# Performance work log

Hardware: AMD Instinct MI355X
Metric: run time of the kernel (lower is better)

The kernel has to match this reference:

```python
import jax, jax.numpy as jnp
import numpy as np

B, C, H, W = 8, 512, 64, 64
HEADS, GROUPS, EPS = 4, 32, 1e-5


def setup_inputs() -> dict:
    key = jax.random.key(0)
    ks = jax.random.split(key, 7)
    s = 0.02
    return {
        "x": jax.random.normal(ks[0], (B, C, H, W), dtype=jnp.float32),
        "gn_w": jnp.ones((C,), dtype=jnp.float32),
        "gn_b": jnp.zeros((C,), dtype=jnp.float32),
        "qkv_w": jax.random.normal(ks[1], (3 * C, C), dtype=jnp.float32) * s,
        "qkv_b": jnp.zeros((3 * C,), dtype=jnp.float32),
        "proj_w": jax.random.normal(ks[2], (C, C), dtype=jnp.float32) * s,
        "proj_b": jnp.zeros((C,), dtype=jnp.float32),
    }


def reference(x, gn_w, gn_b, qkv_w, qkv_b, proj_w, proj_b):
    b, c, h, w = x.shape
    d = c // HEADS  # per-head channel dim
    n = h * w
    # GroupNorm(32, C)
    xg = x.reshape(b, GROUPS, -1)
    mu = xg.mean(axis=-1, keepdims=True)
    var = xg.var(axis=-1, keepdims=True)
    hn = ((xg - mu) * jax.lax.rsqrt(var + EPS)).reshape(b, c, h, w)
    hn = hn * gn_w[:, None, None] + gn_b[:, None, None]
    # 1x1 conv qkv: [3C, C] contraction over channels
    qkv = jnp.einsum('oc,bchw->bohw', qkv_w, hn) + qkv_b[:, None, None]
    qkv = qkv.reshape(b, 3, HEADS, d, n)
    q, k, v = qkv[:, 0], qkv[:, 1], qkv[:, 2]  # each [b, heads, d, n]
    # NOTE: as in the source, q @ k^T contracts over spatial dim -> [b,heads,d,d]
    attn = jnp.einsum('bhdn,bhen->bhde', q, k) * (d ** -0.5)
    attn = jax.nn.softmax(attn, axis=-1)
    out = jnp.einsum('bhde,bhen->bhdn', attn, v).reshape(b, c, h, w)
    out = jnp.einsum('oc,bchw->bohw', proj_w, out) + proj_b[:, None, None]
    return x + out
```

## Files before the change

### kernel.cpp

```cpp
#include <hip/hip_runtime.h>
#include <hip/hip_bf16.h>

typedef __hip_bfloat16 bf16;
typedef __bf16 v8bf __attribute__((ext_vector_type(8)));
typedef float  v4f  __attribute__((ext_vector_type(4)));

struct __align__(8) bf16x4 { bf16 x, y, z, w; };

__device__ __forceinline__ bf16 f2b(float v) { return __float2bfloat16(v); }

#define NSP 4096
#define CCH 512

__device__ __forceinline__ void async_cp16(const bf16* g, __bf16* l) {
    __builtin_amdgcn_global_load_lds(
        (const __attribute__((address_space(1))) unsigned int*)(unsigned long long)g,
        (__attribute__((address_space(3))) unsigned int*)(unsigned int)(unsigned long long)l,
        16, 0, 0);
}

__global__ __launch_bounds__(256) void wconv_kernel(const float* __restrict__ src,
                                                    bf16* __restrict__ dst, int n4) {
    int i = blockIdx.x * 256 + threadIdx.x;
    if (i < n4) {
        float4 v = ((const float4*)src)[i];
        bf16x4 o = { f2b(v.x), f2b(v.y), f2b(v.z), f2b(v.w) };
        ((bf16x4*)dst)[i] = o;
    }
}

__global__ __launch_bounds__(256) void gn_stats_kernel(const float* __restrict__ x,
                                                       float* __restrict__ stats) {
    int blk = blockIdx.x;
    int b = blk >> 5, g = blk & 31;
    size_t base = ((size_t)(b * CCH + g * 16)) * NSP;
    const float4* xp4 = (const float4*)(x + base);
    int t = threadIdx.x;
    float s = 0.f, s2 = 0.f;
    for (int i = t; i < 16384; i += 256) {
        float4 v = xp4[i];
        s  += v.x + v.y + v.z + v.w;
        s2 += v.x * v.x + v.y * v.y + v.z * v.z + v.w * v.w;
    }
    for (int off = 32; off > 0; off >>= 1) {
        s  += __shfl_down(s, off);
        s2 += __shfl_down(s2, off);
    }
    __shared__ float red[8];
    int wid = t >> 6, lid = t & 63;
    if (lid == 0) { red[wid] = s; red[wid + 4] = s2; }
    __syncthreads();
    if (t == 0) {
        float ts  = red[0] + red[1] + red[2] + red[3];
        float ts2 = red[4] + red[5] + red[6] + red[7];
        float mean = ts * (1.f / 65536.f);
        float var  = ts2 * (1.f / 65536.f) - mean * mean;
        stats[blk * 2]     = mean;
        stats[blk * 2 + 1] = rsqrtf(var + 1e-5f);
    }
}

__global__ __launch_bounds__(256) void gn_norm_t_kernel(const float* __restrict__ x,
                                                        const float* __restrict__ gw,
                                                        const float* __restrict__ gb,
                                                        const float* __restrict__ stats,
                                                        bf16* __restrict__ hnT) {
    __shared__ float sT[64][65];
    int n0 = blockIdx.x * 64, c0 = blockIdx.y * 64, b = blockIdx.z;
    int t = threadIdx.x;
    int cl = t >> 4, nl4 = (t & 15) << 2;
#pragma unroll
    for (int it = 0; it < 4; ++it) {
        int crow = cl + it * 16;
        int c = c0 + crow;
        int bg = b * 32 + (c >> 4);
        float mean = stats[bg * 2], rstd = stats[bg * 2 + 1];
        float wsc = gw[c] * rstd;
        float bb  = gb[c] - mean * wsc;
        float4 v = *(const float4*)&x[((long)b * CCH + c) * NSP + n0 + nl4];
        sT[crow][nl4 + 0] = v.x * wsc + bb;
        sT[crow][nl4 + 1] = v.y * wsc + bb;
        sT[crow][nl4 + 2] = v.z * wsc + bb;
        sT[crow][nl4 + 3] = v.w * wsc + bb;
    }
    __syncthreads();
    int nl = t >> 4, cl4 = (t & 15) << 2;
#pragma unroll
    for (int it = 0; it < 4; ++it) {
        int nrow = nl + it * 16;
        bf16x4 ov = { f2b(sT[cl4 + 0][nrow]), f2b(sT[cl4 + 1][nrow]),
                      f2b(sT[cl4 + 2][nrow]), f2b(sT[cl4 + 3][nrow]) };
        *(bf16x4*)&hnT[((long)b * NSP + n0 + nrow) * CCH + c0 + cl4] = ov;
    }
}

__device__ __forceinline__ void gemm_core(const bf16* __restrict__ A, long as,
                                          const bf16* __restrict__ B, long bs,
                                          int K, v4f acc[4][4],
                                          __bf16* sA, __bf16* sB) {
    int t = threadIdx.x;
    int lane = t & 63, wv = t >> 6;
    int wr = wv >> 1, wc = wv & 1;
    int lq = lane & 15, quad = lane >> 4;
    int r0 = wv * 16 + (lane >> 2);
    int koff = (lane & 3) * 8;
    __bf16* ldsA0 = sA + wv * 512 + lane * 8;
    __bf16* ldsA1 = ldsA0 + 2048;
    __bf16* ldsB0 = sB + wv * 512 + lane * 8;
    __bf16* ldsB1 = ldsB0 + 2048;
    const __bf16* aBase = sA + (wr * 64) * 32;
    const __bf16* bBase = sB + (wc * 64) * 32;

    for (int k0 = 0; k0 < K; k0 += 32) {
        __syncthreads();
        async_cp16(A + (long)r0 * as + k0 + koff,        ldsA0);
        async_cp16(A + (long)(r0 + 64) * as + k0 + koff, ldsA1);
        async_cp16(B + (long)r0 * bs + k0 + koff,        ldsB0);
        async_cp16(B + (long)(r0 + 64) * bs + k0 + koff, ldsB1);
        __syncthreads();
        v8bf a[4], bf[4];
#pragma unroll
        for (int i = 0; i < 4; ++i)
            a[i] = *(const v8bf*)(aBase + (i * 16 + lq) * 32 + quad * 8);
#pragma unroll
        for (int j = 0; j < 4; ++j)
            bf[j] = *(const v8bf*)(bBase + (j * 16 + lq) * 32 + quad * 8);
#pragma unroll
        for (int i = 0; i < 4; ++i)
#pragma unroll
            for (int j = 0; j < 4; ++j)
                acc[i][j] = __builtin_amdgcn_mfma_f32_16x16x32_bf16(a[i], bf[j], acc[i][j], 0, 0, 0);
    }
}

__device__ __forceinline__ void gemm256_core(const bf16* __restrict__ A, long lda,
                                             const bf16* __restrict__ B, long ldb,
                                             int K, v4f acc[8][4], char* sLds) {
    const int t = threadIdx.x;
    const int lane = t & 63, wv = t >> 6;
    const int wm = wv >> 2, wn = wv & 3;
    const int lq = lane & 15, quad = lane >> 4;
    const int xsw = (lq & 7) << 4;
    const int kq0 = ((quad << 4)) ^ xsw;
    const int kq1 = (64 | (quad << 4)) ^ xsw;
    const int aRow0 = (wm * 128 + lq) << 7;
    const int bRow0 = (wn * 64 + lq) << 7;
    const int NT = K >> 6;

    auto STAGE = [&](const bf16* mb, long ld, int ldsbyte, int ktile, int h) {
#pragma unroll
        for (int s = 0; s < 2; ++s) {
            int L = (s << 13) + (t << 4);
            int row = L >> 7;
            int kb = (L & 127) ^ ((row & 7) << 4);
            const char* g = (const char*)(mb + (long)(h * 128 + row) * ld + (long)ktile * 64);
            async_cp16((const bf16*)(g + kb),
                       (__bf16*)(sLds + ldsbyte + (h << 14) + L));
        }
    };

    STAGE(B, ldb, 32768, 0, 0);
    STAGE(B, ldb, 32768, 0, 1);
    STAGE(A, lda, 0,     0, 0);
    STAGE(A, lda, 0,     0, 1);
    if (NT > 1) {
        STAGE(B, ldb, 65536 + 32768, 1, 0);
        STAGE(B, ldb, 65536 + 32768, 1, 1);
        asm volatile("s_waitcnt vmcnt(4)" ::: "memory");
    } else {
        asm volatile("s_waitcnt vmcnt(0)" ::: "memory");
    }
    __builtin_amdgcn_s_barrier();
    asm volatile("" ::: "memory");

    for (int kt = 0; kt < NT; ++kt) {
        const int cb = (kt & 1) << 16;
        const int nb = cb ^ 65536;
        const int bufA = cb, bufB = cb | 32768;
        v8bf a[4][2], b0[2][2], b1[2][2];

#pragma unroll
        for (int ii = 0; ii < 4; ++ii) {
            a[ii][0] = *(const v8bf*)(sLds + bufA + aRow0 + ((ii * 16) << 7) + kq0);
            a[ii][1] = *(const v8bf*)(sLds + bufA + aRow0 + ((ii * 16) << 7) + kq1);
        }
#pragma unroll
        for (int jj = 0; jj < 2; ++jj) {
            b0[jj][0] = *(const v8bf*)(sLds + bufB + bRow0 + ((jj * 16) << 7) + kq0);
            b0[jj][1] = *(const v8bf*)(sLds + bufB + bRow0 + ((jj * 16) << 7) + kq1);
        }
        if (kt + 1 < NT) STAGE(A, lda, nb, kt + 1, 0);
        __builtin_amdgcn_s_setprio(1);
#pragma unroll
        for (int ii = 0; ii < 4; ++ii)
#pragma unroll
            for (int jj = 0; jj < 2; ++jj) {
                acc[ii][jj] = __builtin_amdgcn_mfma_f32_16x16x32_bf16(a[ii][0], b0[jj][0], acc[ii][jj], 0, 0, 0);
                acc[ii][jj] = __builtin_amdgcn_mfma_f32_16x16x32_bf16(a[ii][1], b0[jj][1], acc[ii][jj], 0, 0, 0);
            }
        __builtin_amdgcn_s_setprio(0);
        __builtin_amdgcn_s_barrier();
        asm volatile("" ::: "memory");

#pragma unroll
        for (int jj = 0; jj < 2; ++jj) {
            b1[jj][0] = *(const v8bf*)(sLds + bufB + bRow0 + ((32 + jj * 16) << 7) + kq0);
            b1[jj][1] = *(const v8bf*)(sLds + bufB + bRow0 + ((32 + jj * 16) << 7) + kq1);
        }
        if (kt + 1 < NT) STAGE(A, lda, nb, kt + 1, 1);
        __builtin_amdgcn_s_setprio(1);
#pragma unroll
        for (int ii = 0; ii < 4; ++ii)
#pragma unroll
            for (int jj = 0; jj < 2; ++jj) {
                acc[ii][2 + jj] = __builtin_amdgcn_mfma_f32_16x16x32_bf16(a[ii][0], b1[jj][0], acc[ii][2 + jj], 0, 0, 0);
                acc[ii][2 + jj] = __builtin_amdgcn_mfma_f32_16x16x32_bf16(a[ii][1], b1[jj][1], acc[ii][2 + jj], 0, 0, 0);
            }
        __builtin_amdgcn_s_setprio(0);
        __builtin_amdgcn_s_barrier();
        asm volatile("" ::: "memory");

#pragma unroll
        for (int ii = 0; ii < 4; ++ii) {
            a[ii][0] = *(const v8bf*)(sLds + bufA + aRow0 + ((64 + ii * 16) << 7) + kq0);
            a[ii][1] = *(const v8bf*)(sLds + bufA + aRow0 + ((64 + ii * 16) << 7) + kq1);
        }
        if (kt + 2 < NT) STAGE(B, ldb, bufB, kt + 2, 0);
        __builtin_amdgcn_s_setprio(1);
#pragma unroll
        for (int ii = 0; ii < 4; ++ii)
#pragma unroll
            for (int jj = 0; jj < 2; ++jj) {
                acc[4 + ii][2 + jj] = __builtin_amdgcn_mfma_f32_16x16x32_bf16(a[ii][0], b1[jj][0], acc[4 + ii][2 + jj], 0, 0, 0);
                acc[4 + ii][2 + jj] = __builtin_amdgcn_mfma_f32_16x16x32_bf16(a[ii][1], b1[jj][1], acc[4 + ii][2 + jj], 0, 0, 0);
            }
        __builtin_amdgcn_s_setprio(0);
        __builtin_amdgcn_s_barrier();
        asm volatile("" ::: "memory");

        if (kt + 2 < NT) STAGE(B, ldb, bufB, kt + 2, 1);
        __builtin_amdgcn_s_setprio(1);
#pragma unroll
        for (int ii = 0; ii < 4; ++ii)
#pragma unroll
            for (int jj = 0; jj < 2; ++jj) {
                acc[4 + ii][jj] = __builtin_amdgcn_mfma_f32_16x16x32_bf16(a[ii][0], b0[jj][0], acc[4 + ii][jj], 0, 0, 0);
                acc[4 + ii][jj] = __builtin_amdgcn_mfma_f32_16x16x32_bf16(a[ii][1], b0[jj][1], acc[4 + ii][jj], 0, 0, 0);
            }
        __builtin_amdgcn_s_setprio(0);
        if (kt + 2 < NT) asm volatile("s_waitcnt vmcnt(4)" ::: "memory");
        else             asm volatile("s_waitcnt vmcnt(0)" ::: "memory");
        __builtin_amdgcn_s_barrier();
        asm volatile("" ::: "memory");
    }
}

__global__ __launch_bounds__(512, 2) void qkv_gemm_kernel(const bf16* __restrict__ hnT,
                                                          const bf16* __restrict__ qkv_wb,
                                                          const float* __restrict__ qkv_b,
                                                          bf16* __restrict__ qkbuf,
                                                          bf16* __restrict__ vT) {
    __shared__ __align__(16) char sLds[131072];
    int n0 = blockIdx.x * 256, o0 = blockIdx.y * 256, b = blockIdx.z;
    v4f acc[8][4] = {};
    gemm256_core(hnT + ((long)b * NSP + n0) * CCH, CCH,
                 qkv_wb + (long)o0 * CCH, CCH, CCH, acc, sLds);
    int t = threadIdx.x, lane = t & 63, wv = t >> 6, wm = wv >> 2, wn = wv & 3;
    int lq = lane & 15, quad = lane >> 4;
    if (o0 < 1024) {
#pragma unroll
        for (int j = 0; j < 4; ++j) {
            int o = o0 + wn * 64 + j * 16 + lq;
            float bias = qkv_b[o];
#pragma unroll
            for (int i = 0; i < 8; ++i) {
                int n = n0 + wm * 128 + i * 16 + quad * 4;
                v4f v = acc[i][j];
                bf16x4 ov = { f2b(v[0] + bias), f2b(v[1] + bias),
                              f2b(v[2] + bias), f2b(v[3] + bias) };
                *(bf16x4*)&qkbuf[((long)b * 1024 + o) * NSP + n] = ov;
            }
        }
    } else {
#pragma unroll
        for (int j = 0; j < 4; ++j) {
            int e = o0 - 1024 + wn * 64 + j * 16 + lq;
            float bias = qkv_b[1024 + e];
#pragma unroll
            for (int i = 0; i < 8; ++i) {
                int n = n0 + wm * 128 + i * 16 + quad * 4;
                v4f v = acc[i][j];
#pragma unroll
                for (int r = 0; r < 4; ++r)
                    vT[((long)b * NSP + n + r) * CCH + e] = f2b(v[r] + bias);
            }
        }
    }
}

__global__ __launch_bounds__(256) void qk_gemm_kernel(const bf16* __restrict__ qkbuf,
                                                      float* __restrict__ P_part) {
    __shared__ __align__(16) __bf16 sA[128 * 32];
    __shared__ __align__(16) __bf16 sB[128 * 32];
    int s = blockIdx.x, bh = blockIdx.y;
    int b = bh >> 2, h = bh & 3;
    const bf16* q  = qkbuf + ((long)b * 1024 + h * 128) * NSP + s * 512;
    const bf16* kk = qkbuf + ((long)b * 1024 + 512 + h * 128) * NSP + s * 512;
    v4f acc[4][4] = {};
    gemm_core(q, NSP, kk, NSP, 512, acc, sA, sB);
    float* Pp = P_part + ((long)s * 32 + bh) * 16384;
    int t = threadIdx.x, lane = t & 63, wv = t >> 6, wr = wv >> 1, wc = wv & 1;
    int lq = lane & 15, quad = lane >> 4;
#pragma unroll
    for (int j = 0; j < 4; ++j) {
        int e = wc * 64 + j * 16 + lq;
#pragma unroll
        for (int i = 0; i < 4; ++i) {
            int d = wr * 64 + i * 16 + quad * 4;
            v4f v = acc[i][j];
#pragma unroll
            for (int r = 0; r < 4; ++r) Pp[(long)(d + r) * 128 + e] = v[r];
        }
    }
}

__global__ __launch_bounds__(128) void softmax_kernel(const float* __restrict__ P_part,
                                                      bf16* __restrict__ Pb) {
    int row = blockIdx.x;
    int bh = row >> 7, d = row & 127;
    int t = threadIdx.x;
    float v = 0.f;
#pragma unroll
    for (int s = 0; s < 8; ++s)
        v += P_part[((long)s * 32 + bh) * 16384 + (long)d * 128 + t];
    v *= 0.08838834764831845f;
    float m = v;
    for (int off = 32; off > 0; off >>= 1) m = fmaxf(m, __shfl_down(m, off));
    __shared__ float sm[2];
    if ((t & 63) == 0) sm[t >> 6] = m;
    __syncthreads();
    m = fmaxf(sm[0], sm[1]);
    float e = __expf(v - m);
    float ssum = e;
    for (int off = 32; off > 0; off >>= 1) ssum += __shfl_down(ssum, off);
    __shared__ float ss[2];
    if ((t & 63) == 0) ss[t >> 6] = ssum;
    __syncthreads();
    ssum = ss[0] + ss[1];
    Pb[(long)row * 128 + t] = f2b(e / ssum);
}

__global__ __launch_bounds__(256) void pv_gemm_kernel(const bf16* __restrict__ Pb,
                                                      const bf16* __restrict__ vT,
                                                      bf16* __restrict__ attT) {
    __shared__ __align__(16) char sV[2][32768];
    int ng = blockIdx.x, bh = blockIdx.y;
    int b = bh >> 2, h = bh & 3;
    int t = threadIdx.x, lane = t & 63, wv = t >> 6, wr = wv >> 1, wc = wv & 1;
    int lq = lane & 15, quad = lane >> 4;

    auto STAGEV = [&](int n0, int buf) {
#pragma unroll
        for (int s = 0; s < 8; ++s) {
            int L = (s << 12) + (t << 4);
            int row = L >> 8;
            int col = (L & 255) ^ ((row & 7) << 4);
            async_cp16((const bf16*)((const char*)(vT + ((long)b * NSP + n0 + row) * CCH + h * 128) + col),
                       (__bf16*)(&sV[buf][0] + L));
        }
    };

    int n00 = ng * 256;
    STAGEV(n00, 0);
    v8bf a[4][4];
    const char* Pp = (const char*)(Pb + (long)bh * 16384);
#pragma unroll
    for (int i = 0; i < 4; ++i)
#pragma unroll
        for (int ks = 0; ks < 4; ++ks)
            a[i][ks] = *(const v8bf*)(Pp + ((wr * 64 + i * 16 + lq) << 8) + (ks << 6) + (quad << 4));
    STAGEV(n00 + 128, 1);
    asm volatile("s_waitcnt vmcnt(8)" ::: "memory");
    __syncthreads();

#pragma unroll
    for (int nt = 0; nt < 2; ++nt) {
        int n0 = n00 + nt * 128;
        const char* base = &sV[nt][0];
        v4f acc[4][4] = {};
#pragma unroll
        for (int ks = 0; ks < 4; ++ks) {
            v8bf bv[4];
#pragma unroll
            for (int j = 0; j < 4; ++j) {
                int r = wc * 64 + j * 16 + lq;
                bv[j] = *(const v8bf*)(base + (r << 8) + (((ks << 6) + (quad << 4)) ^ ((r & 7) << 4)));
            }
#pragma unroll
            for (int i = 0; i < 4; ++i)
#pragma unroll
                for (int j = 0; j < 4; ++j)
                    acc[i][j] = __builtin_amdgcn_mfma_f32_16x16x32_bf16(a[i][ks], bv[j], acc[i][j], 0, 0, 0);
        }
#pragma unroll
        for (int j = 0; j < 4; ++j) {
            int n = n0 + wc * 64 + j * 16 + lq;
#pragma unroll
            for (int i = 0; i < 4; ++i) {
                int d = wr * 64 + i * 16 + quad * 4;
                v4f v = acc[i][j];
                bf16x4 ov = { f2b(v[0]), f2b(v[1]), f2b(v[2]), f2b(v[3]) };
                *(bf16x4*)&attT[((long)b * NSP + n) * CCH + h * 128 + d] = ov;
            }
        }
        if (nt == 0) {
            asm volatile("s_waitcnt vmcnt(0)" ::: "memory");
            __syncthreads();
        }
    }
}

__global__ __launch_bounds__(512, 2) void proj_gemm_kernel(const bf16* __restrict__ attT,
                                                           const bf16* __restrict__ proj_wb,
                                                           const float* __restrict__ proj_b,
                                                           const float* __restrict__ x,
                                                           float* __restrict__ out) {
    __shared__ __align__(16) char sLds[131072];
    int n0 = blockIdx.x * 256, c0 = blockIdx.y * 256, b = blockIdx.z;
    v4f acc[8][4] = {};
    gemm256_core(attT + ((long)b * NSP + n0) * CCH, CCH,
                 proj_wb + (long)c0 * CCH, CCH, CCH, acc, sLds);
    int t = threadIdx.x, lane = t & 63, wv = t >> 6, wm = wv >> 2, wn = wv & 3;
    int lq = lane & 15, quad = lane >> 4;
#pragma unroll
    for (int j = 0; j < 4; ++j) {
        int c = c0 + wn * 64 + j * 16 + lq;
        float bias = proj_b[c];
#pragma unroll
        for (int i = 0; i < 8; ++i) {
            int n = n0 + wm * 128 + i * 16 + quad * 4;
            long idx = ((long)b * CCH + c) * NSP + n;
            float4 r = *(const float4*)&x[idx];
            v4f v = acc[i][j];
            float4 ov = { v[0] + bias + r.x, v[1] + bias + r.y,
                          v[2] + bias + r.z, v[3] + bias + r.w };
            *(float4*)&out[idx] = ov;
        }
    }
}

extern "C" void kernel_launch(void* const* d_in, const int* in_sizes, int n_in,
                              void* d_out, int out_size, void* d_ws, size_t ws_size,
                              hipStream_t stream) {
    const float* x      = (const float*)d_in[0];
    const float* gn_w   = (const float*)d_in[1];
    const float* gn_b   = (const float*)d_in[2];
    const float* qkv_w  = (const float*)d_in[3];
    const float* qkv_b  = (const float*)d_in[4];
    const float* proj_w = (const float*)d_in[5];
    const float* proj_b = (const float*)d_in[6];
    float* out = (float*)d_out;

    char* ws = (char*)d_ws;
    bf16*  hnT    = (bf16*)ws;
    float* P_part = (float*)ws;
    bf16*  attT   = (bf16*)ws;
    bf16*  qkbuf  = (bf16*)(ws + 33554432);
    bf16*  vT     = (bf16*)(ws + 100663296);
    bf16*  Pb     = (bf16*)(ws + 134217728);
    float* stats  = (float*)(ws + 135266304);
    bf16*  qkv_wb = (bf16*)(ws + 135270400);
    bf16*  proj_wb= (bf16*)(ws + 136843264);

    wconv_kernel<<<768, 256, 0, stream>>>(qkv_w, qkv_wb, 196608);
    wconv_kernel<<<256, 256, 0, stream>>>(proj_w, proj_wb, 65536);
    gn_stats_kernel<<<256, 256, 0, stream>>>(x, stats);
    gn_norm_t_kernel<<<dim3(64, 8, 8), 256, 0, stream>>>(x, gn_w, gn_b, stats, hnT);
    qkv_gemm_kernel<<<dim3(16, 6, 8), 512, 0, stream>>>(hnT, qkv_wb, qkv_b, qkbuf, vT);
    qk_gemm_kernel<<<dim3(8, 32), 256, 0, stream>>>(qkbuf, P_part);
    softmax_kernel<<<4096, 128, 0, stream>>>(P_part, Pb);
    pv_gemm_kernel<<<dim3(16, 32), 256, 0, stream>>>(Pb, vT, attT);
    proj_gemm_kernel<<<dim3(16, 2, 8), 512, 0, stream>>>(attT, proj_wb, proj_b, x, out);
}
```

Measured before the change: 307.4 us.

## Make QKV GEMM persistent with three tiles per block and cross-tile prefetch

The QKV GEMM launch changes from a 768-block grid to 256 persistent blocks, each computing three consecutive 256x256 output tiles. The K-loop pipeline is inlined and keeps prefetching across tile boundaries, so the next tile's first A/B k-tiles load while the current tile finishes. The goal is to remove per-tile pipeline warm-up and drain and to avoid a partial last wave across the 256 CUs. The cost is a longer serial chain per block, and the epilogue stores are not overlapped with the loads.

```diff
diff --git a/kernel.cpp b/kernel.cpp
--- a/kernel.cpp
+++ b/kernel.cpp
@@ -261,38 +261,188 @@
                                                           bf16* __restrict__ qkbuf,
                                                           bf16* __restrict__ vT) {
     __shared__ __align__(16) char sLds[131072];
-    int n0 = blockIdx.x * 256, o0 = blockIdx.y * 256, b = blockIdx.z;
+    const int p = blockIdx.x;
+    const int t = threadIdx.x;
+    const int lane = t & 63, wv = t >> 6;
+    const int wm = wv >> 2, wn = wv & 3;
+    const int lq = lane & 15, quad = lane >> 4;
+    const int xsw = (lq & 7) << 4;
+    const int kq0 = ((quad << 4)) ^ xsw;
+    const int kq1 = (64 | (quad << 4)) ^ xsw;
+    const int aRow0 = (wm * 128 + lq) << 7;
+    const int bRow0 = (wn * 64 + lq) << 7;
+
+    auto decodeA = [&](int l) -> const bf16* {
+        int n0 = (l & 15) << 8; int b = (l >> 4) / 6;
+        return hnT + ((long)b * NSP + n0) * CCH;
+    };
+    auto decodeB = [&](int l) -> const bf16* {
+        int o0 = ((l >> 4) % 6) << 8;
+        return qkv_wb + (long)o0 * CCH;
+    };
+
+    auto STAGE = [&](const bf16* mb, int ldsbyte, int ktile, int h) {
+#pragma unroll
+        for (int s = 0; s < 2; ++s) {
+            int L = (s << 13) + (t << 4);
+            int row = L >> 7;
+            int kb = (L & 127) ^ ((row & 7) << 4);
+            const char* g = (const char*)(mb + (long)(h * 128 + row) * CCH + (long)ktile * 64);
+            async_cp16((const bf16*)(g + kb),
+                       (__bf16*)(sLds + ldsbyte + (h << 14) + L));
+        }
+    };
+
+    const int l0 = p * 3;
+    const bf16* Acur = decodeA(l0);
+    const bf16* Bcur = decodeB(l0);
+    const bf16* Anxt = decodeA(l0 + 1);
+    const bf16* Bnxt = decodeB(l0 + 1);
+
     v4f acc[8][4] = {};
-    gemm256_core(hnT + ((long)b * NSP + n0) * CCH, CCH,
-                 qkv_wb + (long)o0 * CCH, CCH, CCH, acc, sLds);
-    int t = threadIdx.x, lane = t & 63, wv = t >> 6, wm = wv >> 2, wn = wv & 3;
-    int lq = lane & 15, quad = lane >> 4;
-    if (o0 < 1024) {
-#pragma unroll
-        for (int j = 0; j < 4; ++j) {
-            int o = o0 + wn * 64 + j * 16 + lq;
-            float bias = qkv_b[o];
-#pragma unroll
-            for (int i = 0; i < 8; ++i) {
-                int n = n0 + wm * 128 + i * 16 + quad * 4;
-                v4f v = acc[i][j];
-                bf16x4 ov = { f2b(v[0] + bias), f2b(v[1] + bias),
-                              f2b(v[2] + bias), f2b(v[3] + bias) };
-                *(bf16x4*)&qkbuf[((long)b * 1024 + o) * NSP + n] = ov;
-            }
-        }
-    } else {
-#pragma unroll
-        for (int j = 0; j < 4; ++j) {
-            int e = o0 - 1024 + wn * 64 + j * 16 + lq;
-            float bias = qkv_b[1024 + e];
-#pragma unroll
-            for (int i = 0; i < 8; ++i) {
-                int n = n0 + wm * 128 + i * 16 + quad * 4;
-                v4f v = acc[i][j];
-#pragma unroll
-                for (int r = 0; r < 4; ++r)
-                    vT[((long)b * NSP + n + r) * CCH + e] = f2b(v[r] + bias);
+
+    STAGE(Bcur, 32768, 0, 0);
+    STAGE(Bcur, 32768, 0, 1);
+    STAGE(Acur, 0,     0, 0);
+    STAGE(Acur, 0,     0, 1);
+    STAGE(Bcur, 65536 + 32768, 1, 0);
+    STAGE(Bcur, 65536 + 32768, 1, 1);
+    asm volatile("s_waitcnt vmcnt(4)" ::: "memory");
+    __builtin_amdgcn_s_barrier();
+    asm volatile("" ::: "memory");
+
+    for (int ti = 0; ti < 3; ++ti) {
+        for (int kt = 0; kt < 8; ++kt) {
+            const int cb = (kt & 1) << 16;
+            const int nb = cb ^ 65536;
+            const int bufA = cb, bufB = cb | 32768;
+            v8bf a[4][2], b0[2][2], b1[2][2];
+
+            const bf16* As = (kt < 7) ? Acur : Anxt;
+            const int   Akt = (kt < 7) ? kt + 1 : 0;
+            const bool  doA = !(ti == 2 && kt == 7);
+            const bf16* Bs = (kt < 6) ? Bcur : Bnxt;
+            const int   Bkt = (kt < 6) ? kt + 2 : kt - 6;
+            const bool  doB = !(ti == 2 && kt >= 6);
+
+#pragma unroll
+            for (int ii = 0; ii < 4; ++ii) {
+                a[ii][0] = *(const v8bf*)(sLds + bufA + aRow0 + ((ii * 16) << 7) + kq0);
+                a[ii][1] = *(const v8bf*)(sLds + bufA + aRow0 + ((ii * 16) << 7) + kq1);
+            }
+#pragma unroll
+            for (int jj = 0; jj < 2; ++jj) {
+                b0[jj][0] = *(const v8bf*)(sLds + bufB + bRow0 + ((jj * 16) << 7) + kq0);
+                b0[jj][1] = *(const v8bf*)(sLds + bufB + bRow0 + ((jj * 16) << 7) + kq1);
+            }
+            if (doA) STAGE(As, nb, Akt, 0);
+            __builtin_amdgcn_s_setprio(1);
+#pragma unroll
+            for (int ii = 0; ii < 4; ++ii)
+#pragma unroll
+                for (int jj = 0; jj < 2; ++jj) {
+                    acc[ii][jj] = __builtin_amdgcn_mfma_f32_16x16x32_bf16(a[ii][0], b0[jj][0], acc[ii][jj], 0, 0, 0);
+                    acc[ii][jj] = __builtin_amdgcn_mfma_f32_16x16x32_bf16(a[ii][1], b0[jj][1], acc[ii][jj], 0, 0, 0);
+                }
+            __builtin_amdgcn_s_setprio(0);
+            __builtin_amdgcn_s_barrier();
+            asm volatile("" ::: "memory");
+
+#pragma unroll
+            for (int jj = 0; jj < 2; ++jj) {
+                b1[jj][0] = *(const v8bf*)(sLds + bufB + bRow0 + ((32 + jj * 16) << 7) + kq0);
+                b1[jj][1] = *(const v8bf*)(sLds + bufB + bRow0 + ((32 + jj * 16) << 7) + kq1);
+            }
+            if (doA) STAGE(As, nb, Akt, 1);
+            __builtin_amdgcn_s_setprio(1);
+#pragma unroll
+            for (int ii = 0; ii < 4; ++ii)
+#pragma unroll
+                for (int jj = 0; jj < 2; ++jj) {
+                    acc[ii][2 + jj] = __builtin_amdgcn_mfma_f32_16x16x32_bf16(a[ii][0], b1[jj][0], acc[ii][2 + jj], 0, 0, 0);
+                    acc[ii][2 + jj] = __builtin_amdgcn_mfma_f32_16x16x32_bf16(a[ii][1], b1[jj][1], acc[ii][2 + jj], 0, 0, 0);
+                }
+            __builtin_amdgcn_s_setprio(0);
+            __builtin_amdgcn_s_barrier();
+            asm volatile("" ::: "memory");
+
+#pragma unroll
+            for (int ii = 0; ii < 4; ++ii) {
+                a[ii][0] = *(const v8bf*)(sLds + bufA + aRow0 + ((64 + ii * 16) << 7) + kq0);
+                a[ii][1] = *(const v8bf*)(sLds + bufA + aRow0 + ((64 + ii * 16) << 7) + kq1);
+            }
+            if (doB) STAGE(Bs, bufB, Bkt, 0);
+            __builtin_amdgcn_s_setprio(1);
+#pragma unroll
+            for (int ii = 0; ii < 4; ++ii)
+#pragma unroll
+                for (int jj = 0; jj < 2; ++jj) {
+                    acc[4 + ii][2 + jj] = __builtin_amdgcn_mfma_f32_16x16x32_bf16(a[ii][0], b1[jj][0], acc[4 + ii][2 + jj], 0, 0, 0);
+                    acc[4 + ii][2 + jj] = __builtin_amdgcn_mfma_f32_16x16x32_bf16(a[ii][1], b1[jj][1], acc[4 + ii][2 + jj], 0, 0, 0);
+                }
+            __builtin_amdgcn_s_setprio(0);
+            __builtin_amdgcn_s_barrier();
+            asm volatile("" ::: "memory");
+
+            if (doB) STAGE(Bs, bufB, Bkt, 1);
+            __builtin_amdgcn_s_setprio(1);
+#pragma unroll
+            for (int ii = 0; ii < 4; ++ii)
+#pragma unroll
+                for (int jj = 0; jj < 2; ++jj) {
+                    acc[4 + ii][jj] = __builtin_amdgcn_mfma_f32_16x16x32_bf16(a[ii][0], b0[jj][0], acc[4 + ii][jj], 0, 0, 0);
+                    acc[4 + ii][jj] = __builtin_amdgcn_mfma_f32_16x16x32_bf16(a[ii][1], b0[jj][1], acc[4 + ii][jj], 0, 0, 0);
+                }
+            __builtin_amdgcn_s_setprio(0);
+            if (doB) asm volatile("s_waitcnt vmcnt(4)" ::: "memory");
+            else     asm volatile("s_waitcnt vmcnt(0)" ::: "memory");
+            __builtin_amdgcn_s_barrier();
+            asm volatile("" ::: "memory");
+        }
+
+        {
+            int l = l0 + ti;
+            int n0 = (l & 15) << 8;
+            int oc = l >> 4;
+            int o0 = (oc % 6) << 8;
+            int b  = oc / 6;
+            if (o0 < 1024) {
+#pragma unroll
+                for (int j = 0; j < 4; ++j) {
+                    int o = o0 + wn * 64 + j * 16 + lq;
+                    float bias = qkv_b[o];
+#pragma unroll
+                    for (int i = 0; i < 8; ++i) {
+                        int n = n0 + wm * 128 + i * 16 + quad * 4;
+                        v4f v = acc[i][j];
+                        bf16x4 ov = { f2b(v[0] + bias), f2b(v[1] + bias),
+                                      f2b(v[2] + bias), f2b(v[3] + bias) };
+                        *(bf16x4*)&qkbuf[((long)b * 1024 + o) * NSP + n] = ov;
+                    }
+                }
+            } else {
+#pragma unroll
+                for (int j = 0; j < 4; ++j) {
+                    int e = o0 - 1024 + wn * 64 + j * 16 + lq;
+                    float bias = qkv_b[1024 + e];
+#pragma unroll
+                    for (int i = 0; i < 8; ++i) {
+                        int n = n0 + wm * 128 + i * 16 + quad * 4;
+                        v4f v = acc[i][j];
+#pragma unroll
+                        for (int r = 0; r < 4; ++r)
+                            vT[((long)b * NSP + n + r) * CCH + e] = f2b(v[r] + bias);
+                    }
+                }
+            }
+            if (ti < 2) {
+#pragma unroll
+                for (int i = 0; i < 8; ++i)
+#pragma unroll
+                    for (int j = 0; j < 4; ++j)
+                        acc[i][j] = (v4f){0.f, 0.f, 0.f, 0.f};
+                Acur = Anxt; Bcur = Bnxt;
+                if (ti == 0) { Anxt = decodeA(l0 + 2); Bnxt = decodeB(l0 + 2); }
             }
         }
     }
@@ -476,7 +626,7 @@
     wconv_kernel<<<256, 256, 0, stream>>>(proj_w, proj_wb, 65536);
     gn_stats_kernel<<<256, 256, 0, stream>>>(x, stats);
     gn_norm_t_kernel<<<dim3(64, 8, 8), 256, 0, stream>>>(x, gn_w, gn_b, stats, hnT);
-    qkv_gemm_kernel<<<dim3(16, 6, 8), 512, 0, stream>>>(hnT, qkv_wb, qkv_b, qkbuf, vT);
+    qkv_gemm_kernel<<<256, 512, 0, stream>>>(hnT, qkv_wb, qkv_b, qkbuf, vT);
     qk_gemm_kernel<<<dim3(8, 32), 256, 0, stream>>>(qkbuf, P_part);
     softmax_kernel<<<4096, 128, 0, stream>>>(P_part, Pb);
     pv_gemm_kernel<<<dim3(16, 32), 256, 0, stream>>>(Pb, vT, attT);
```

Result: slower. 350.3 us (+13.9%).
